# Optimization experiments

Measured on AMD Instinct MI355X. Metric: run time of the kernel, lower is better.

The kernel has to match this reference:

```python
import jax, jax.numpy as jnp
import numpy as np

EMBED = 1024
HEAD = 128

def setup_inputs() -> dict:
    key = jax.random.key(0)
    k1, k2, k3, k4 = jax.random.split(key, 4)
    x = jax.random.normal(k1, (4, 4096, EMBED), dtype=jnp.float32)
    # nn.Linear default init ~ U(-1/sqrt(fan_in), 1/sqrt(fan_in)); weights stored as [in, out] for x @ W
    s = 1.0 / np.sqrt(EMBED)
    Wq = jax.random.uniform(k2, (EMBED, HEAD), dtype=jnp.float32, minval=-s, maxval=s)
    Wk = jax.random.uniform(k3, (EMBED, HEAD), dtype=jnp.float32, minval=-s, maxval=s)
    Wv = jax.random.uniform(k4, (EMBED, HEAD), dtype=jnp.float32, minval=-s, maxval=s)
    return {"x": x, "Wq": Wq, "Wk": Wk, "Wv": Wv}

def reference(x, Wq, Wk, Wv):
    # x: [B, S, E]
    B, S, E = x.shape
    q = x @ Wq  # [B, S, H]
    k = x @ Wk
    v = x @ Wv
    scale = jnp.asarray(k.shape[-1], x.dtype) ** -0.5
    scores = jnp.einsum('bqh,bkh->bqk', q, k) * scale  # [B, S, S]
    causal = jnp.tril(jnp.ones((S, S), dtype=bool))
    scores = jnp.where(causal, scores, jnp.asarray(-jnp.inf, x.dtype))
    attn = jax.nn.softmax(scores, axis=-1)
    return jnp.einsum('bqk,bkh->bqh', attn, v)  # [B, S, H]
```

## Files before the change

### kernel.cpp

```cpp
#include <hip/hip_runtime.h>
#include <math.h>

#define BATCH 4
#define SEQ   4096
#define EMB   1024
#define HD    128
#define MROWS (BATCH*SEQ)
#define SCALE 0.08838834764831844f
#define CHUNK 10
#define NJOBS 119
#define MAXC  7

typedef __attribute__((ext_vector_type(8))) short bf16x8;
typedef __attribute__((ext_vector_type(4))) short short4v;
typedef __attribute__((ext_vector_type(4))) float f32x4;
typedef __attribute__((ext_vector_type(4))) int   i32x4;

static __device__ __forceinline__ unsigned short f2bf(float f) {
    unsigned int u = __float_as_uint(f);
    u += 0x7fff + ((u >> 16) & 1);
    return (unsigned short)(u >> 16);
}
static __device__ __forceinline__ float bf2f(unsigned short s) {
    return __uint_as_float((unsigned int)s << 16);
}

__global__ __launch_bounds__(256) void wtrans_kernel(
    const float* __restrict__ Wq, const float* __restrict__ Wk,
    const float* __restrict__ Wv, unsigned short* __restrict__ Wt)
{
    __shared__ __align__(16) unsigned short Xs[16 * 132];
    const int w  = blockIdx.y;
    const float* W = (w == 0) ? Wq : (w == 1) ? Wk : Wv;
    const float sc = (w == 0) ? SCALE : 1.0f;
    unsigned short* dst = Wt + (size_t)w * 131072;
    const int k0 = blockIdx.x * 16;
    const int t  = threadIdx.x;

#pragma unroll
    for (int i = 0; i < 2; ++i) {
        int gg = i * 256 + t;
        int row = gg >> 5, c4 = gg & 31;
        float4 a = *(const float4*)&W[(size_t)(k0 + row) * HD + c4 * 4];
        short4v p;
        p[0] = (short)f2bf(a.x * sc); p[1] = (short)f2bf(a.y * sc);
        p[2] = (short)f2bf(a.z * sc); p[3] = (short)f2bf(a.w * sc);
        *(short4v*)&Xs[row * 132 + c4 * 4] = p;
    }
    __syncthreads();
    const int n = t >> 1, half = t & 1;
    i32x4 o;
#pragma unroll
    for (int e = 0; e < 4; ++e) {
        unsigned int lo = Xs[(half * 8 + e * 2    ) * 132 + n];
        unsigned int hi = Xs[(half * 8 + e * 2 + 1) * 132 + n];
        o[e] = (int)(lo | (hi << 16));
    }
    *(i32x4*)&dst[(size_t)n * 1024 + k0 + half * 8] = o;
}

__global__ __launch_bounds__(512, 4) void qkv_kernel(
    const float* __restrict__ x, const unsigned short* __restrict__ Wt,
    unsigned short* __restrict__ qb, unsigned short* __restrict__ kb,
    unsigned short* __restrict__ vtb)
{
    __shared__ __align__(16) unsigned short lds[2 * 2304 + 384 * 72];
    unsigned short* xs0 = lds;
    unsigned short* xs1 = lds + 2304;
    unsigned short* Ws  = lds + 4608;

    const int t    = threadIdx.x;
    const int lane = t & 63, ng = t >> 6;
    const int quad = lane >> 4, l16 = lane & 15;
    const int m0   = blockIdx.x * 32;

    f32x4 acc[2][3];
#pragma unroll
    for (int i = 0; i < 2; ++i)
#pragma unroll
        for (int j = 0; j < 3; ++j) acc[i][j] = (f32x4){0.f, 0.f, 0.f, 0.f};

    const int xrow = t >> 3, xseg = t & 7;
    if (t < 256) {
        float4 a = *(const float4*)&x[(size_t)(m0 + xrow) * EMB + xseg * 8];
        float4 b2 = *(const float4*)&x[(size_t)(m0 + xrow) * EMB + xseg * 8 + 4];
        i32x4 p;
        p[0] = (int)((unsigned)f2bf(a.x) | ((unsigned)f2bf(a.y) << 16));
        p[1] = (int)((unsigned)f2bf(a.z) | ((unsigned)f2bf(a.w) << 16));
        p[2] = (int)((unsigned)f2bf(b2.x) | ((unsigned)f2bf(b2.y) << 16));
        p[3] = (int)((unsigned)f2bf(b2.z) | ((unsigned)f2bf(b2.w) << 16));
        *(i32x4*)&xs0[xrow * 72 + xseg * 8] = p;
    }
    __syncthreads();

    for (int kt = 0; kt < EMB; kt += 64) {
        unsigned short* xb = (kt & 64) ? xs1 : xs0;
        unsigned short* xn = (kt & 64) ? xs0 : xs1;
#pragma unroll
        for (int i = 0; i < 6; ++i) {
            int rowl = ng * 48 + i * 8 + (lane >> 3);
            int seg  = lane & 7;
            *(i32x4*)&Ws[rowl * 72 + seg * 8] =
                *(const i32x4*)&Wt[(size_t)rowl * 1024 + kt + seg * 8];
        }
        if (t < 256 && kt + 64 < EMB) {
            float4 a = *(const float4*)&x[(size_t)(m0 + xrow) * EMB + kt + 64 + xseg * 8];
            float4 b2 = *(const float4*)&x[(size_t)(m0 + xrow) * EMB + kt + 64 + xseg * 8 + 4];
            i32x4 p;
            p[0] = (int)((unsigned)f2bf(a.x) | ((unsigned)f2bf(a.y) << 16));
            p[1] = (int)((unsigned)f2bf(a.z) | ((unsigned)f2bf(a.w) << 16));
            p[2] = (int)((unsigned)f2bf(b2.x) | ((unsigned)f2bf(b2.y) << 16));
            p[3] = (int)((unsigned)f2bf(b2.z) | ((unsigned)f2bf(b2.w) << 16));
            *(i32x4*)&xn[xrow * 72 + xseg * 8] = p;
        }
#pragma unroll
        for (int ks = 0; ks < 2; ++ks) {
            bf16x8 aA[2], aB[3];
#pragma unroll
            for (int mt = 0; mt < 2; ++mt)
                aA[mt] = *(const bf16x8*)&xb[(mt * 16 + l16) * 72 + ks * 32 + quad * 8];
#pragma unroll
            for (int jt = 0; jt < 3; ++jt)
                aB[jt] = *(const bf16x8*)&Ws[((ng * 3 + jt) * 16 + l16) * 72 + ks * 32 + quad * 8];
#pragma unroll
            for (int mt = 0; mt < 2; ++mt)
#pragma unroll
                for (int jt = 0; jt < 3; ++jt)
                    acc[mt][jt] = __builtin_amdgcn_mfma_f32_16x16x32_bf16(
                        aA[mt], aB[jt], acc[mt][jt], 0, 0, 0);
        }
        __syncthreads();
    }

    unsigned short* Cq = lds;
    unsigned short* Ck = lds + 32 * 136;
    unsigned short* Cv = lds + 2 * 32 * 136;
#pragma unroll
    for (int mt = 0; mt < 2; ++mt)
#pragma unroll
        for (int jt = 0; jt < 3; ++jt) {
            int nt = ng * 3 + jt;
            int wm = nt >> 3, nl = nt & 7;
            if (wm < 2) {
                unsigned short* C = (wm == 0) ? Cq : Ck;
#pragma unroll
                for (int rr = 0; rr < 4; ++rr)
                    C[(mt * 16 + quad * 4 + rr) * 136 + nl * 16 + l16] =
                        f2bf(acc[mt][jt][rr]);
            } else {
                short4v p;
                p[0] = (short)f2bf(acc[mt][jt][0]); p[1] = (short)f2bf(acc[mt][jt][1]);
                p[2] = (short)f2bf(acc[mt][jt][2]); p[3] = (short)f2bf(acc[mt][jt][3]);
                *(short4v*)&Cv[(nl * 16 + l16) * 40 + mt * 16 + quad * 4] = p;
            }
        }
    __syncthreads();
    {
        int row = t >> 4, seg = t & 15;
        *(i32x4*)&qb[((size_t)(m0 + row)) * HD + seg * 8] = *(const i32x4*)&Cq[row * 136 + seg * 8];
        *(i32x4*)&kb[((size_t)(m0 + row)) * HD + seg * 8] = *(const i32x4*)&Ck[row * 136 + seg * 8];
    }
    {
        const int b = m0 >> 12, s0 = m0 & 4095;
        int h = t >> 2, seg = t & 3;
        *(i32x4*)&vtb[(size_t)b * (HD * SEQ) + (size_t)h * SEQ + s0 + seg * 8] =
            *(const i32x4*)&Cv[h * 40 + seg * 8];
    }
}

#define PADK 136
#define PADV 72
#define PADP 72

__global__ __launch_bounds__(512, 4) void flash_kernel(
    const unsigned short* __restrict__ qb, const unsigned short* __restrict__ kb,
    const unsigned short* __restrict__ vtb, unsigned short* __restrict__ Opart,
    float* __restrict__ mbuf, float* __restrict__ lbuf)
{
    __shared__ __align__(16) unsigned short Ks[64 * PADK];
    __shared__ __align__(16) unsigned short Vt[128 * PADV];
    __shared__ __align__(16) unsigned short Pt[128 * PADP];

    const int bx   = blockIdx.x;
    const int slot = bx & 7, pp = bx >> 3;
    const int b    = slot >> 1;
    const int jj   = pp * 2 + (slot & 1);
    if (jj >= NJOBS) return;

    const int t    = threadIdx.x;
    const int lane = t & 63, w = t >> 6;
    const int quad = lane >> 4, l16 = lane & 15;

    int qi = 0, s = 0;
    for (qi = 0; qi < 32; ++qi) {
        int cnt = (qi + 5) / 5;
        if (jj < s + cnt) break;
        s += cnt;
    }
    const int c    = jj - s;
    const int qrow = qi * 128 + w * 16 + l16;
    const int jmax = 2 * qi + 2;
    const int jbeg = c * CHUNK;
    const int jend = min(jbeg + CHUNK, jmax);

    bf16x8 qf[4];
    {
        const unsigned short* qp = qb + ((size_t)b * SEQ + qrow) * HD;
#pragma unroll
        for (int ks = 0; ks < 4; ++ks)
            qf[ks] = *(const bf16x8*)&qp[ks * 32 + quad * 8];
    }

    f32x4 O[8];
#pragma unroll
    for (int i = 0; i < 8; ++i) O[i] = (f32x4){0.f, 0.f, 0.f, 0.f};
    float m_run = -1e30f, l_run = 0.f;

    const unsigned short* kbb  = kb  + (size_t)b * SEQ * HD;
    const unsigned short* vtbb = vtb + (size_t)b * HD * SEQ;

    for (int j0 = jbeg; j0 < jend; ++j0) {
        __syncthreads();
#pragma unroll
        for (int i = 0; i < 2; ++i) {
            int gg = i * 512 + t;
            i32x4 kd = *(const i32x4*)&kbb[(size_t)j0 * 64 * HD + (size_t)gg * 8];
            *(i32x4*)&Ks[(gg >> 4) * PADK + (gg & 15) * 8] = kd;
        }
#pragma unroll
        for (int i = 0; i < 2; ++i) {
            int gg = i * 512 + t;
            i32x4 vd = *(const i32x4*)&vtbb[(size_t)(gg >> 3) * SEQ + j0 * 64 + (gg & 7) * 8];
            *(i32x4*)&Vt[(gg >> 3) * PADV + (gg & 7) * 8] = vd;
        }
        __syncthreads();

        if (j0 * 64 > qi * 128 + w * 16 + 15) continue;

        f32x4 st[4];
#pragma unroll
        for (int mt = 0; mt < 4; ++mt) {
            f32x4 a = (f32x4){0.f, 0.f, 0.f, 0.f};
#pragma unroll
            for (int ks = 0; ks < 4; ++ks) {
                bf16x8 kf = *(const bf16x8*)&Ks[(mt * 16 + l16) * PADK + ks * 32 + quad * 8];
                a = __builtin_amdgcn_mfma_f32_16x16x32_bf16(kf, qf[ks], a, 0, 0, 0);
            }
            st[mt] = a;
        }

        if (j0 * 64 + 63 > qi * 128 + w * 16) {
#pragma unroll
            for (int mt = 0; mt < 4; ++mt)
#pragma unroll
                for (int rr = 0; rr < 4; ++rr) {
                    int kv = j0 * 64 + mt * 16 + quad * 4 + rr;
                    if (kv > qrow) st[mt][rr] = -1e30f;
                }
        }

        float mx = -1e30f;
#pragma unroll
        for (int mt = 0; mt < 4; ++mt)
#pragma unroll
            for (int rr = 0; rr < 4; ++rr) mx = fmaxf(mx, st[mt][rr]);
        mx = fmaxf(mx, __shfl_xor(mx, 16));
        mx = fmaxf(mx, __shfl_xor(mx, 32));
        const float m_new = fmaxf(m_run, mx);
        const float alpha = __expf(m_run - m_new);
        float psum = 0.f;
#pragma unroll
        for (int mt = 0; mt < 4; ++mt)
#pragma unroll
            for (int rr = 0; rr < 4; ++rr) {
                float p = __expf(st[mt][rr] - m_new);
                st[mt][rr] = p;
                psum += p;
            }
        psum += __shfl_xor(psum, 16);
        psum += __shfl_xor(psum, 32);
        m_run = m_new;
        l_run = l_run * alpha + psum;

#pragma unroll
        for (int mt = 0; mt < 4; ++mt) {
            short4v p;
            p[0] = (short)f2bf(st[mt][0]); p[1] = (short)f2bf(st[mt][1]);
            p[2] = (short)f2bf(st[mt][2]); p[3] = (short)f2bf(st[mt][3]);
            *(short4v*)&Pt[(w * 16 + l16) * PADP + mt * 16 + quad * 4] = p;
        }

#pragma unroll
        for (int i = 0; i < 8; ++i) {
            O[i][0] *= alpha; O[i][1] *= alpha; O[i][2] *= alpha; O[i][3] *= alpha;
        }

        bf16x8 pf0 = *(const bf16x8*)&Pt[(w * 16 + l16) * PADP + quad * 8];
        bf16x8 pf1 = *(const bf16x8*)&Pt[(w * 16 + l16) * PADP + 32 + quad * 8];
#pragma unroll
        for (int mt = 0; mt < 8; ++mt) {
            bf16x8 vf0 = *(const bf16x8*)&Vt[(mt * 16 + l16) * PADV + quad * 8];
            bf16x8 vf1 = *(const bf16x8*)&Vt[(mt * 16 + l16) * PADV + 32 + quad * 8];
            O[mt] = __builtin_amdgcn_mfma_f32_16x16x32_bf16(vf0, pf0, O[mt], 0, 0, 0);
            O[mt] = __builtin_amdgcn_mfma_f32_16x16x32_bf16(vf1, pf1, O[mt], 0, 0, 0);
        }
    }

    const int r = w * 16 + l16;
    const size_t jobbase = (size_t)b * NJOBS + jj;
    unsigned short* po = Opart + jobbase * (128 * 128) + (size_t)r * 128;
#pragma unroll
    for (int mt = 0; mt < 8; ++mt) {
        short4v p;
        p[0] = (short)f2bf(O[mt][0]); p[1] = (short)f2bf(O[mt][1]);
        p[2] = (short)f2bf(O[mt][2]); p[3] = (short)f2bf(O[mt][3]);
        *(short4v*)&po[mt * 16 + quad * 4] = p;
    }
    if (quad == 0) {
        mbuf[jobbase * 128 + r] = m_run;
        lbuf[jobbase * 128 + r] = l_run;
    }
}

__global__ __launch_bounds__(512) void combine_kernel(
    const unsigned short* __restrict__ Opart, const float* __restrict__ mbuf,
    const float* __restrict__ lbuf, float* __restrict__ out)
{
    const int qi = blockIdx.x, b = blockIdx.y;
    const int nc = (qi + 5) / 5;
    int j0 = 0;
    for (int q = 0; q < qi; ++q) j0 += (q + 5) / 5;
    const int t = threadIdx.x;
    const int row = t >> 2, cg = (t & 3) * 32;

    float mv[MAXC], lv[MAXC];
    float M = -1e30f;
#pragma unroll
    for (int c2 = 0; c2 < MAXC; ++c2) {
        if (c2 < nc) {
            const size_t jb = (size_t)b * NJOBS + j0 + c2;
            mv[c2] = mbuf[jb * 128 + row];
            lv[c2] = lbuf[jb * 128 + row];
            M = fmaxf(M, mv[c2]);
        } else { mv[c2] = -1e30f; lv[c2] = 0.f; }
    }
    float L = 0.f;
#pragma unroll
    for (int c2 = 0; c2 < MAXC; ++c2)
        if (c2 < nc) L += __expf(mv[c2] - M) * lv[c2];
    const float Linv = 1.0f / L;

    float acc[32];
#pragma unroll
    for (int i = 0; i < 32; ++i) acc[i] = 0.f;
#pragma unroll
    for (int c2 = 0; c2 < MAXC; ++c2) {
        if (c2 < nc) {
            const float wgt = __expf(mv[c2] - M) * Linv;
            const unsigned short* po = Opart + ((size_t)b * NJOBS + j0 + c2) * (128 * 128) +
                                       (size_t)row * 128 + cg;
#pragma unroll
            for (int i = 0; i < 4; ++i) {
                i32x4 d = *(const i32x4*)&po[i * 8];
#pragma unroll
                for (int e = 0; e < 4; ++e) {
                    unsigned int u = (unsigned int)d[e];
                    acc[i * 8 + e * 2]     = fmaf(wgt, bf2f((unsigned short)(u & 0xffff)), acc[i * 8 + e * 2]);
                    acc[i * 8 + e * 2 + 1] = fmaf(wgt, bf2f((unsigned short)(u >> 16)),   acc[i * 8 + e * 2 + 1]);
                }
            }
        }
    }
    float* op = out + ((size_t)b * SEQ + qi * 128 + row) * HD + cg;
#pragma unroll
    for (int i = 0; i < 8; ++i) {
        float4 res;
        res.x = acc[i * 4]; res.y = acc[i * 4 + 1];
        res.z = acc[i * 4 + 2]; res.w = acc[i * 4 + 3];
        *(float4*)&op[i * 4] = res;
    }
}

extern "C" void kernel_launch(void* const* d_in, const int* in_sizes, int n_in,
                              void* d_out, int out_size, void* d_ws, size_t ws_size,
                              hipStream_t stream) {
    const float* x  = (const float*)d_in[0];
    const float* Wq = (const float*)d_in[1];
    const float* Wk = (const float*)d_in[2];
    const float* Wv = (const float*)d_in[3];

    unsigned short* qb    = (unsigned short*)d_ws;
    unsigned short* kb    = qb  + (size_t)MROWS * HD;
    unsigned short* vtb   = kb  + (size_t)MROWS * HD;
    unsigned short* Wt    = vtb + (size_t)MROWS * HD;
    unsigned short* Opart = Wt  + (size_t)3 * HD * EMB;
    float* mbuf = (float*)(Opart + (size_t)BATCH * NJOBS * 128 * 128);
    float* lbuf = mbuf + (size_t)BATCH * NJOBS * 128;
    float* out = (float*)d_out;

    wtrans_kernel <<<dim3(64, 3),  dim3(256), 0, stream>>>(Wq, Wk, Wv, Wt);
    qkv_kernel    <<<dim3(512),    dim3(512), 0, stream>>>(x, Wt, qb, kb, vtb);
    flash_kernel  <<<dim3(480),    dim3(512), 0, stream>>>(qb, kb, vtb, Opart, mbuf, lbuf);
    combine_kernel<<<dim3(32, 4),  dim3(512), 0, stream>>>(Opart, mbuf, lbuf, out);
}
```

Baseline: 168.4 us.

## Prefetch K/V into registers, defer softmax rescale, use exp2 and MFMA priority

The Q weights are pre-scaled by scale*log2(e) so the softmax can use exp2f in place of __expf. Softmax rescaling of O and l is skipped until the row max grows past a threshold. The flash kernel now loads the next K/V tile into registers while the current tile is computed, and s_setprio raises wave priority around MFMA blocks. The QKV projection drops its LDS staging of W, reads weight fragments straight from global memory, and has all 512 threads convert x. Together these aim to hide load latency and cut exp and rescale ALU work, at the cost of extra registers, uncoalesced global W reads, and a bounded risk of overflow from deferred rescaling.

```diff
diff --git a/kernel.cpp b/kernel.cpp
--- a/kernel.cpp
+++ b/kernel.cpp
@@ -6,7 +6,8 @@
 #define EMB   1024
 #define HD    128
 #define MROWS (BATCH*SEQ)
-#define SCALE 0.08838834764831844f
+#define SCALE  0.08838834764831844f
+#define SCALEQ 0.12751742f
 #define CHUNK 10
 #define NJOBS 119
 #define MAXC  7
@@ -32,7 +33,7 @@
     __shared__ __align__(16) unsigned short Xs[16 * 132];
     const int w  = blockIdx.y;
     const float* W = (w == 0) ? Wq : (w == 1) ? Wk : Wv;
-    const float sc = (w == 0) ? SCALE : 1.0f;
+    const float sc = (w == 0) ? SCALEQ : 1.0f;
     unsigned short* dst = Wt + (size_t)w * 131072;
     const int k0 = blockIdx.x * 16;
     const int t  = threadIdx.x;
@@ -64,10 +65,9 @@
     unsigned short* __restrict__ qb, unsigned short* __restrict__ kb,
     unsigned short* __restrict__ vtb)
 {
-    __shared__ __align__(16) unsigned short lds[2 * 2304 + 384 * 72];
+    __shared__ __align__(16) unsigned short lds[13824];
     unsigned short* xs0 = lds;
     unsigned short* xs1 = lds + 2304;
-    unsigned short* Ws  = lds + 4608;
 
     const int t    = threadIdx.x;
     const int lane = t & 63, ng = t >> 6;
@@ -80,55 +80,49 @@
 #pragma unroll
         for (int j = 0; j < 3; ++j) acc[i][j] = (f32x4){0.f, 0.f, 0.f, 0.f};
 
-    const int xrow = t >> 3, xseg = t & 7;
-    if (t < 256) {
-        float4 a = *(const float4*)&x[(size_t)(m0 + xrow) * EMB + xseg * 8];
-        float4 b2 = *(const float4*)&x[(size_t)(m0 + xrow) * EMB + xseg * 8 + 4];
-        i32x4 p;
-        p[0] = (int)((unsigned)f2bf(a.x) | ((unsigned)f2bf(a.y) << 16));
-        p[1] = (int)((unsigned)f2bf(a.z) | ((unsigned)f2bf(a.w) << 16));
-        p[2] = (int)((unsigned)f2bf(b2.x) | ((unsigned)f2bf(b2.y) << 16));
-        p[3] = (int)((unsigned)f2bf(b2.z) | ((unsigned)f2bf(b2.w) << 16));
-        *(i32x4*)&xs0[xrow * 72 + xseg * 8] = p;
+    const int xrow = t >> 4, xseg = t & 15;
+    {
+        float4 a = *(const float4*)&x[(size_t)(m0 + xrow) * EMB + xseg * 4];
+        short4v p;
+        p[0] = (short)f2bf(a.x); p[1] = (short)f2bf(a.y);
+        p[2] = (short)f2bf(a.z); p[3] = (short)f2bf(a.w);
+        *(short4v*)&xs0[xrow * 72 + xseg * 4] = p;
     }
     __syncthreads();
+
+    const unsigned short* Wb = Wt + ((size_t)(ng * 48 + l16)) * 1024 + quad * 8;
 
     for (int kt = 0; kt < EMB; kt += 64) {
         unsigned short* xb = (kt & 64) ? xs1 : xs0;
         unsigned short* xn = (kt & 64) ? xs0 : xs1;
-#pragma unroll
-        for (int i = 0; i < 6; ++i) {
-            int rowl = ng * 48 + i * 8 + (lane >> 3);
-            int seg  = lane & 7;
-            *(i32x4*)&Ws[rowl * 72 + seg * 8] =
-                *(const i32x4*)&Wt[(size_t)rowl * 1024 + kt + seg * 8];
-        }
-        if (t < 256 && kt + 64 < EMB) {
-            float4 a = *(const float4*)&x[(size_t)(m0 + xrow) * EMB + kt + 64 + xseg * 8];
-            float4 b2 = *(const float4*)&x[(size_t)(m0 + xrow) * EMB + kt + 64 + xseg * 8 + 4];
-            i32x4 p;
-            p[0] = (int)((unsigned)f2bf(a.x) | ((unsigned)f2bf(a.y) << 16));
-            p[1] = (int)((unsigned)f2bf(a.z) | ((unsigned)f2bf(a.w) << 16));
-            p[2] = (int)((unsigned)f2bf(b2.x) | ((unsigned)f2bf(b2.y) << 16));
-            p[3] = (int)((unsigned)f2bf(b2.z) | ((unsigned)f2bf(b2.w) << 16));
-            *(i32x4*)&xn[xrow * 72 + xseg * 8] = p;
-        }
-#pragma unroll
-        for (int ks = 0; ks < 2; ++ks) {
-            bf16x8 aA[2], aB[3];
+        if (kt + 64 < EMB) {
+            float4 a = *(const float4*)&x[(size_t)(m0 + xrow) * EMB + kt + 64 + xseg * 4];
+            short4v p;
+            p[0] = (short)f2bf(a.x); p[1] = (short)f2bf(a.y);
+            p[2] = (short)f2bf(a.z); p[3] = (short)f2bf(a.w);
+            *(short4v*)&xn[xrow * 72 + xseg * 4] = p;
+        }
+        bf16x8 aB[2][3], aA[2][2];
+#pragma unroll
+        for (int ks = 0; ks < 2; ++ks)
+#pragma unroll
+            for (int jt = 0; jt < 3; ++jt)
+                aB[ks][jt] = *(const bf16x8*)&Wb[(size_t)jt * 16 * 1024 + kt + ks * 32];
+#pragma unroll
+        for (int ks = 0; ks < 2; ++ks)
 #pragma unroll
             for (int mt = 0; mt < 2; ++mt)
-                aA[mt] = *(const bf16x8*)&xb[(mt * 16 + l16) * 72 + ks * 32 + quad * 8];
-#pragma unroll
-            for (int jt = 0; jt < 3; ++jt)
-                aB[jt] = *(const bf16x8*)&Ws[((ng * 3 + jt) * 16 + l16) * 72 + ks * 32 + quad * 8];
+                aA[ks][mt] = *(const bf16x8*)&xb[(mt * 16 + l16) * 72 + ks * 32 + quad * 8];
+        __builtin_amdgcn_s_setprio(1);
+#pragma unroll
+        for (int ks = 0; ks < 2; ++ks)
 #pragma unroll
             for (int mt = 0; mt < 2; ++mt)
 #pragma unroll
                 for (int jt = 0; jt < 3; ++jt)
                     acc[mt][jt] = __builtin_amdgcn_mfma_f32_16x16x32_bf16(
-                        aA[mt], aB[jt], acc[mt][jt], 0, 0, 0);
-        }
+                        aA[ks][mt], aB[ks][jt], acc[mt][jt], 0, 0, 0);
+        __builtin_amdgcn_s_setprio(0);
         __syncthreads();
     }
 
@@ -171,6 +165,7 @@
 #define PADK 136
 #define PADV 72
 #define PADP 72
+#define DEFER_THR 8.0f
 
 __global__ __launch_bounds__(512, 4) void flash_kernel(
     const unsigned short* __restrict__ qb, const unsigned short* __restrict__ kb,
@@ -202,6 +197,7 @@
     const int jmax = 2 * qi + 2;
     const int jbeg = c * CHUNK;
     const int jend = min(jbeg + CHUNK, jmax);
+    const int wtop = qi * 128 + w * 16;
 
     bf16x8 qf[4];
     {
@@ -219,25 +215,33 @@
     const unsigned short* kbb  = kb  + (size_t)b * SEQ * HD;
     const unsigned short* vtbb = vtb + (size_t)b * HD * SEQ;
 
+    const int gg0 = t, gg1 = 512 + t;
+    i32x4 kr0, kr1, vr0, vr1;
+    kr0 = *(const i32x4*)&kbb[(size_t)jbeg * 64 * HD + (size_t)gg0 * 8];
+    kr1 = *(const i32x4*)&kbb[(size_t)jbeg * 64 * HD + (size_t)gg1 * 8];
+    vr0 = *(const i32x4*)&vtbb[(size_t)(gg0 >> 3) * SEQ + jbeg * 64 + (gg0 & 7) * 8];
+    vr1 = *(const i32x4*)&vtbb[(size_t)(gg1 >> 3) * SEQ + jbeg * 64 + (gg1 & 7) * 8];
+
     for (int j0 = jbeg; j0 < jend; ++j0) {
         __syncthreads();
-#pragma unroll
-        for (int i = 0; i < 2; ++i) {
-            int gg = i * 512 + t;
-            i32x4 kd = *(const i32x4*)&kbb[(size_t)j0 * 64 * HD + (size_t)gg * 8];
-            *(i32x4*)&Ks[(gg >> 4) * PADK + (gg & 15) * 8] = kd;
-        }
-#pragma unroll
-        for (int i = 0; i < 2; ++i) {
-            int gg = i * 512 + t;
-            i32x4 vd = *(const i32x4*)&vtbb[(size_t)(gg >> 3) * SEQ + j0 * 64 + (gg & 7) * 8];
-            *(i32x4*)&Vt[(gg >> 3) * PADV + (gg & 7) * 8] = vd;
-        }
+        *(i32x4*)&Ks[(gg0 >> 4) * PADK + (gg0 & 15) * 8] = kr0;
+        *(i32x4*)&Ks[(gg1 >> 4) * PADK + (gg1 & 15) * 8] = kr1;
+        *(i32x4*)&Vt[(gg0 >> 3) * PADV + (gg0 & 7) * 8] = vr0;
+        *(i32x4*)&Vt[(gg1 >> 3) * PADV + (gg1 & 7) * 8] = vr1;
         __syncthreads();
 
-        if (j0 * 64 > qi * 128 + w * 16 + 15) continue;
+        if (j0 + 1 < jend) {
+            const int j1 = j0 + 1;
+            kr0 = *(const i32x4*)&kbb[(size_t)j1 * 64 * HD + (size_t)gg0 * 8];
+            kr1 = *(const i32x4*)&kbb[(size_t)j1 * 64 * HD + (size_t)gg1 * 8];
+            vr0 = *(const i32x4*)&vtbb[(size_t)(gg0 >> 3) * SEQ + j1 * 64 + (gg0 & 7) * 8];
+            vr1 = *(const i32x4*)&vtbb[(size_t)(gg1 >> 3) * SEQ + j1 * 64 + (gg1 & 7) * 8];
+        }
+
+        if (j0 * 64 > wtop + 15) continue;
 
         f32x4 st[4];
+        __builtin_amdgcn_s_setprio(1);
 #pragma unroll
         for (int mt = 0; mt < 4; ++mt) {
             f32x4 a = (f32x4){0.f, 0.f, 0.f, 0.f};
@@ -248,8 +252,9 @@
             }
             st[mt] = a;
         }
-
-        if (j0 * 64 + 63 > qi * 128 + w * 16) {
+        __builtin_amdgcn_s_setprio(0);
+
+        if (j0 * 64 + 63 > wtop) {
 #pragma unroll
             for (int mt = 0; mt < 4; ++mt)
 #pragma unroll
@@ -266,21 +271,28 @@
             for (int rr = 0; rr < 4; ++rr) mx = fmaxf(mx, st[mt][rr]);
         mx = fmaxf(mx, __shfl_xor(mx, 16));
         mx = fmaxf(mx, __shfl_xor(mx, 32));
-        const float m_new = fmaxf(m_run, mx);
-        const float alpha = __expf(m_run - m_new);
+        if (!__all(mx <= m_run + DEFER_THR)) {
+            const float m_new = fmaxf(m_run, mx);
+            const float alpha = exp2f(m_run - m_new);
+            l_run *= alpha;
+#pragma unroll
+            for (int i = 0; i < 8; ++i) {
+                O[i][0] *= alpha; O[i][1] *= alpha; O[i][2] *= alpha; O[i][3] *= alpha;
+            }
+            m_run = m_new;
+        }
         float psum = 0.f;
 #pragma unroll
         for (int mt = 0; mt < 4; ++mt)
 #pragma unroll
             for (int rr = 0; rr < 4; ++rr) {
-                float p = __expf(st[mt][rr] - m_new);
+                float p = exp2f(st[mt][rr] - m_run);
                 st[mt][rr] = p;
                 psum += p;
             }
         psum += __shfl_xor(psum, 16);
         psum += __shfl_xor(psum, 32);
-        m_run = m_new;
-        l_run = l_run * alpha + psum;
+        l_run += psum;
 
 #pragma unroll
         for (int mt = 0; mt < 4; ++mt) {
@@ -290,13 +302,9 @@
             *(short4v*)&Pt[(w * 16 + l16) * PADP + mt * 16 + quad * 4] = p;
         }
 
-#pragma unroll
-        for (int i = 0; i < 8; ++i) {
-            O[i][0] *= alpha; O[i][1] *= alpha; O[i][2] *= alpha; O[i][3] *= alpha;
-        }
-
         bf16x8 pf0 = *(const bf16x8*)&Pt[(w * 16 + l16) * PADP + quad * 8];
         bf16x8 pf1 = *(const bf16x8*)&Pt[(w * 16 + l16) * PADP + 32 + quad * 8];
+        __builtin_amdgcn_s_setprio(1);
 #pragma unroll
         for (int mt = 0; mt < 8; ++mt) {
             bf16x8 vf0 = *(const bf16x8*)&Vt[(mt * 16 + l16) * PADV + quad * 8];
@@ -304,6 +312,7 @@
             O[mt] = __builtin_amdgcn_mfma_f32_16x16x32_bf16(vf0, pf0, O[mt], 0, 0, 0);
             O[mt] = __builtin_amdgcn_mfma_f32_16x16x32_bf16(vf1, pf1, O[mt], 0, 0, 0);
         }
+        __builtin_amdgcn_s_setprio(0);
     }
 
     const int r = w * 16 + l16;
@@ -347,7 +356,7 @@
     float L = 0.f;
 #pragma unroll
     for (int c2 = 0; c2 < MAXC; ++c2)
-        if (c2 < nc) L += __expf(mv[c2] - M) * lv[c2];
+        if (c2 < nc) L += exp2f(mv[c2] - M) * lv[c2];
     const float Linv = 1.0f / L;
 
     float acc[32];
@@ -356,7 +365,7 @@
 #pragma unroll
     for (int c2 = 0; c2 < MAXC; ++c2) {
         if (c2 < nc) {
-            const float wgt = __expf(mv[c2] - M) * Linv;
+            const float wgt = exp2f(mv[c2] - M) * Linv;
             const unsigned short* po = Opart + ((size_t)b * NJOBS + j0 + c2) * (128 * 128) +
                                        (size_t)row * 128 + cg;
 #pragma unroll
```

Result: slower. 190.6 us (+13.2%).
